# Kernel tuning notes

Hardware: AMD Instinct MI355X
Metric: run time of the kernel (lower is better)

The kernel has to match this reference:

```python
import jax, jax.numpy as jnp
import numpy as np

B, N, F, H, HEADS = 2, 256, 64, 64, 4
C = HEADS * H  # n_coefficients (coefficients_mlp is Identity => must equal n_heads*hidden)
EPS = 1e-5
INF = 1e5


def _lin(key, fan_in, fan_out, bias=True):
    k1, k2 = jax.random.split(key)
    w = jax.random.normal(k1, (fan_in, fan_out), jnp.float32) * (1.0 / np.sqrt(fan_in))
    if bias:
        b = jax.random.normal(k2, (fan_out,), jnp.float32) * 0.01
        return w, b
    return w


def setup_inputs() -> dict:
    key = jax.random.key(0)
    ks = jax.random.split(key, 16)
    inp = dict(
        h=jax.random.normal(ks[0], (B, N, F), jnp.float32),
        x=jax.random.normal(ks[1], (B, N, 3), jnp.float32),
        v=jax.random.normal(ks[2], (B, N, 3), jnp.float32),
    )
    inp['edge_w1'], inp['edge_b1'] = _lin(ks[3], 2 * F + 1, H)
    inp['edge_w2'], inp['edge_b2'] = _lin(ks[4], H, H)
    inp['sem_w'], inp['sem_b'] = _lin(ks[5], H, HEADS)
    inp['post_w1'], inp['post_b1'] = _lin(ks[6], C, H)
    inp['post_w2'], inp['post_b2'] = _lin(ks[7], H, H)
    inp['node_w1'], inp['node_b1'] = _lin(ks[8], C + H + F, H)
    inp['node_w2'], inp['node_b2'] = _lin(ks[9], H, F)
    inp['vel_w1'], inp['vel_b1'] = _lin(ks[10], F, H)
    inp['vel_w2'] = _lin(ks[11], H, 1, bias=False) * 0.001  # xavier gain=0.001 analogue
    inp['vmix_w'] = _lin(ks[12], C, 1, bias=False)[:, 0]
    inp['log_gamma'] = -jnp.log(jnp.linspace(1.0, 5.0, HEADS)).astype(jnp.float32)
    return inp


def reference(h, x, v, edge_w1, edge_b1, edge_w2, edge_b2, sem_w, sem_b,
              post_w1, post_b1, post_w2, post_b2, node_w1, node_b1,
              node_w2, node_b2, vel_w1, vel_b1, vel_w2, vmix_w, log_gamma):
    silu = jax.nn.silu
    n = h.shape[-2]
    eye = jnp.eye(n, dtype=h.dtype)[:, :, None]  # [N,N,1] diagonal mask

    # pairwise geometry: entry [i,j] = x_j - x_i
    x_minus_xt = x[..., None, :, :] - x[..., :, None, :]                # [B,N,N,3]
    x_norm = jnp.sqrt((x_minus_xt ** 2).sum(-1, keepdims=True) + EPS)   # [B,N,N,1]

    # pairwise node-feature concat (h_j, h_i) + distance -> edge MLP
    h_j = jnp.broadcast_to(h[..., None, :, :], (B, n, n, F))
    h_i = jnp.broadcast_to(h[..., :, None, :], (B, n, n, F))
    h_cat = jnp.concatenate([h_j, h_i, x_norm], axis=-1)                # [B,N,N,2F+1]
    h_e_mtx = silu(silu(h_cat @ edge_w1 + edge_b1) @ edge_w2 + edge_b2)  # [B,N,N,H]

    # euclidean attention: softmin over j of gamma*dist, diagonal masked out
    dist = (x_norm + INF * eye) * jnp.exp(log_gamma)                    # [B,N,N,heads]
    euclid_att = jax.nn.softmax(-dist, axis=-2)
    # semantic attention: LeakyReLU(0.2) logits, diagonal masked, softmax over j
    sem = jax.nn.leaky_relu(h_e_mtx @ sem_w + sem_b, 0.2) - INF * eye
    sem_att = jax.nn.softmax(sem, axis=-2)
    comb_att = jax.nn.softmax(euclid_att * sem_att, axis=-2)            # [B,N,N,heads]

    # attention-weighted edge features, flattened over (H, heads)
    h_e_att = (h_e_mtx[..., :, None] * comb_att[..., None, :]).reshape(B, n, n, C)

    # spatial attention (coefficients_mlp is Identity)
    unit = x_minus_xt / (x_norm + EPS)                                  # [B,N,N,3]
    # combinations.mean(dim=-3) without materializing [B,N,N,C,3]
    comb_sum = jnp.einsum('bijc,bijd->bicd', h_e_att, unit) / n         # [B,N,C,3]
    comb_norm = (comb_sum ** 2).sum(-1)                                 # [B,N,C]
    h_comb = silu(silu(comb_norm @ post_w1 + post_b1) @ post_w2 + post_b2)

    # delta_v = mean_j (v_mixing over C of combinations)
    delta_v = jnp.einsum('bijc,c,bijd->bid', h_e_att, vmix_w, unit) / n  # [B,N,3]

    h_agg = h_e_att.sum(axis=-2)                                        # sum over j -> [B,N,C]
    out = jnp.concatenate([h, h_agg, h_comb], axis=-1)
    out = silu(silu(out @ node_w1 + node_b1) @ node_w2 + node_b2)
    h_new = h + out                                                     # residual

    # coordinate / velocity update
    v_scale = silu(h_new @ vel_w1 + vel_b1) @ vel_w2                    # [B,N,1]
    v_new = delta_v + v_scale * v
    x_new = x + v_new
    return h_new, x_new, v_new
```

## Files before the change

kernel.cpp:

```cpp
#include <hip/hip_runtime.h>
#include <hip/hip_bf16.h>
#include <math.h>

#define EPSV 1e-5f
#define INFV 1e5f

typedef short bf16x8 __attribute__((ext_vector_type(8)));
typedef float f32x4 __attribute__((ext_vector_type(4)));

__device__ __forceinline__ float rcp_f(float x) { return __builtin_amdgcn_rcpf(x); }
__device__ __forceinline__ float silu_f(float v) { return v * rcp_f(1.0f + __expf(-v)); }

__device__ __forceinline__ unsigned short f2bf(float f) {
  unsigned int u = __float_as_uint(f);
  u = (u + 0x7fffu + ((u >> 16) & 1u)) >> 16;
  return (unsigned short)u;
}
__device__ __forceinline__ float bf2f(unsigned short h) {
  return __uint_as_float(((unsigned int)h) << 16);
}
__device__ __forceinline__ unsigned int pkbf(float a, float b) {
  float2 f2; f2.x = a; f2.y = b;
  __hip_bfloat162 t = __float22bfloat162_rn(f2);
  unsigned int u;
  __builtin_memcpy(&u, &t, 4);
  return u;
}

__device__ __forceinline__ void gemm64(const unsigned short* A_lds, const unsigned short* B_lds,
                                       int w, int l15, int quad, f32x4 acc[4][4]) {
#pragma unroll
  for (int tr = 0; tr < 4; ++tr)
#pragma unroll
    for (int tc = 0; tc < 4; ++tc)
      acc[tr][tc] = (f32x4){0.f, 0.f, 0.f, 0.f};
#pragma unroll
  for (int ms = 0; ms < 64; ms += 32) {
    bf16x8 af[4], bfr[4];
#pragma unroll
    for (int tr = 0; tr < 4; ++tr)
      af[tr] = *reinterpret_cast<const bf16x8*>(&A_lds[(64 * w + 16 * tr + l15) * 72 + ms + quad * 8]);
#pragma unroll
    for (int tc = 0; tc < 4; ++tc)
      bfr[tc] = *reinterpret_cast<const bf16x8*>(&B_lds[(16 * tc + l15) * 72 + ms + quad * 8]);
#pragma unroll
    for (int tr = 0; tr < 4; ++tr)
#pragma unroll
      for (int tc = 0; tc < 4; ++tc)
        acc[tr][tc] = __builtin_amdgcn_mfma_f32_16x16x32_bf16(af[tr], bfr[tc], acc[tr][tc], 0, 0, 0);
  }
}

__global__ __launch_bounds__(512, 2) void k_all(
    const float* __restrict__ h, const float* __restrict__ x, const float* __restrict__ v,
    const float* __restrict__ ew1, const float* __restrict__ eb1,
    const float* __restrict__ ew2, const float* __restrict__ eb2,
    const float* __restrict__ semw, const float* __restrict__ semb,
    const float* __restrict__ pw1, const float* __restrict__ pb1,
    const float* __restrict__ pw2, const float* __restrict__ pb2,
    const float* __restrict__ nw1, const float* __restrict__ nb1,
    const float* __restrict__ nw2, const float* __restrict__ nb2,
    const float* __restrict__ vw1, const float* __restrict__ vb1,
    const float* __restrict__ vw2, const float* __restrict__ vmix,
    const float* __restrict__ lgam, float* __restrict__ out) {

  __shared__ __align__(16) unsigned short TH0[256 * 72];
  __shared__ __align__(16) unsigned short TH1[256 * 72];
  __shared__ __align__(16) char R0[9216];
  __shared__ __align__(16) char R1[9216];
  __shared__ __align__(16) unsigned short E3T[16 * 72];
  __shared__ __align__(16) float4 unit_l[2][256];
  __shared__ float addk[2][64];
  __shared__ float w1dk[64];
  __shared__ __align__(16) float bms[512];

  const int bid = blockIdx.x;
  const int b   = bid >> 7;
  const int ip  = bid & 127;
  const int tid = threadIdx.x;
  const int g   = tid >> 8;
  const int jt  = tid & 255;
  const int i_g = 2 * ip + g;
  const int bi  = (b << 8) | i_g;
  const int bj  = (b << 8) | jt;

  const int w8   = tid >> 6;
  const int lid  = tid & 63;
  const int wg   = w8 & 3;
  const int l15  = lid & 15;
  const int quad = lid >> 4;

  unsigned short* E2Ta = (unsigned short*)R0;
  unsigned short* E2Tb = (unsigned short*)R1;
  unsigned short* THg  = g ? TH1 : TH0;
  char* Rg = g ? R1 : R0;
  float*  sd_g  = (float*)Rg;
  float4* cat_g = (float4*)Rg;
  float*  cn_g  = (float*)(Rg + 4096);
  float*  hag_g = (float*)(Rg + 5120);
  float4* scS   = (float4*)bms + g * 8;
  float4* scP   = (float4*)bms + 16 + g * 4;
  float4* scD   = (float4*)bms + 24 + g * 4;
  float*  dvs_g = bms + 128 + g * 4;

  const float xi0 = x[bi * 3 + 0], xi1 = x[bi * 3 + 1], xi2 = x[bi * 3 + 2];
  const float dx = x[bj * 3 + 0] - xi0;
  const float dy = x[bj * 3 + 1] - xi1;
  const float dz = x[bj * 3 + 2] - xi2;
  const float dn = sqrtf(dx * dx + dy * dy + dz * dz + EPSV);
  const float invn = rcp_f(dn + EPSV);
  const float ux = dx * invn, uy = dy * invn, uz = dz * invn;
  unit_l[g][jt] = make_float4(ux, uy, uz, dn);

  {
    const float4* hb4 = reinterpret_cast<const float4*>(h + (size_t)(b << 8) * 64);
#pragma unroll
    for (int q = 0; q < 8; ++q) {
      int idx = q * 512 + tid;
      float4 f4 = hb4[idx];
      int row = idx >> 4, c4 = idx & 15;
      uint2 pk;
      pk.x = pkbf(f4.x, f4.y);
      pk.y = pkbf(f4.z, f4.w);
      *reinterpret_cast<uint2*>(&TH0[row * 72 + c4 * 4]) = pk;
    }
  }
#pragma unroll
  for (int q = 0; q < 8; ++q) {
    int idx = q * 512 + tid;
    E2Ta[(idx & 63) * 72 + (idx >> 6)] = f2bf(ew1[idx]);
  }
#pragma unroll
  for (int q = 0; q < 8; ++q) {
    int idx = q * 512 + tid;
    E2Tb[(idx & 63) * 72 + (idx >> 6)] = f2bf(ew2[idx]);
  }
  {
    int n = tid >> 6, kk = tid & 63;
    E3T[n * 72 + kk] = f2bf((n < 4) ? semw[kk * 4 + n] : vmix[kk * 4 + (n - 4)]);
    E3T[(8 + n) * 72 + kk] = 0;
  }
  {
    int s = jt >> 6, k = jt & 63;
    const float* hrow = h + (size_t)bi * 64;
    float bp = 0.f;
#pragma unroll
    for (int f2 = 0; f2 < 16; ++f2) {
      int f = s * 16 + f2;
      bp += hrow[f] * ew1[(64 + f) * 64 + k];
    }
    bms[g * 256 + s * 64 + k] = bp;
  }
  __syncthreads();
  if (tid < 128) {
    int ii = tid >> 6, k = tid & 63;
    addk[ii][k] = eb1[k] + bms[ii * 256 + k] + bms[ii * 256 + 64 + k] +
                  bms[ii * 256 + 128 + k] + bms[ii * 256 + 192 + k];
  }
  if (tid < 64) w1dk[tid] = ew1[128 * 64 + tid];

  f32x4 acc1[2][4];
#pragma unroll
  for (int tr = 0; tr < 2; ++tr)
#pragma unroll
    for (int tc = 0; tc < 4; ++tc)
      acc1[tr][tc] = (f32x4){0.f, 0.f, 0.f, 0.f};
#pragma unroll
  for (int ms = 0; ms < 64; ms += 32) {
    bf16x8 af[2], bfr[4];
#pragma unroll
    for (int tr = 0; tr < 2; ++tr)
      af[tr] = *reinterpret_cast<const bf16x8*>(&TH0[(32 * w8 + 16 * tr + l15) * 72 + ms + quad * 8]);
#pragma unroll
    for (int tc = 0; tc < 4; ++tc)
      bfr[tc] = *reinterpret_cast<const bf16x8*>(&E2Ta[(16 * tc + l15) * 72 + ms + quad * 8]);
#pragma unroll
    for (int tr = 0; tr < 2; ++tr)
#pragma unroll
      for (int tc = 0; tc < 4; ++tc)
        acc1[tr][tc] = __builtin_amdgcn_mfma_f32_16x16x32_bf16(af[tr], bfr[tc], acc1[tr][tc], 0, 0, 0);
  }
  __syncthreads();

#pragma unroll
  for (int tc = 0; tc < 4; ++tc) {
    float wd  = w1dk[16 * tc + l15];
    float ak0 = addk[0][16 * tc + l15];
    float ak1 = addk[1][16 * tc + l15];
#pragma unroll
    for (int tr = 0; tr < 2; ++tr)
#pragma unroll
      for (int r = 0; r < 4; ++r) {
        int row = 32 * w8 + 16 * tr + quad * 4 + r;
        float a = acc1[tr][tc][r];
        float d0 = unit_l[0][row].w, d1 = unit_l[1][row].w;
        TH0[row * 72 + 16 * tc + l15] = f2bf(silu_f(a + ak0 + d0 * wd));
        TH1[row * 72 + 16 * tc + l15] = f2bf(silu_f(a + ak1 + d1 * wd));
      }
  }
  __syncthreads();

  f32x4 acc2[4][4];
  gemm64(THg, E2Tb, wg, l15, quad, acc2);
  __syncthreads();
#pragma unroll
  for (int tc = 0; tc < 4; ++tc) {
    float b2 = eb2[16 * tc + l15];
#pragma unroll
    for (int tr = 0; tr < 4; ++tr)
#pragma unroll
      for (int r = 0; r < 4; ++r) {
        int row = 64 * wg + 16 * tr + quad * 4 + r;
        THg[row * 72 + 16 * tc + l15] = f2bf(silu_f(acc2[tr][tc][r] + b2));
      }
  }
  __syncthreads();

  f32x4 acc3[4];
#pragma unroll
  for (int tr = 0; tr < 4; ++tr) acc3[tr] = (f32x4){0.f, 0.f, 0.f, 0.f};
#pragma unroll
  for (int ms = 0; ms < 64; ms += 32) {
    bf16x8 b3 = *reinterpret_cast<const bf16x8*>(&E3T[l15 * 72 + ms + quad * 8]);
#pragma unroll
    for (int tr = 0; tr < 4; ++tr) {
      bf16x8 a3 = *reinterpret_cast<const bf16x8*>(&THg[(64 * wg + 16 * tr + l15) * 72 + ms + quad * 8]);
      acc3[tr] = __builtin_amdgcn_mfma_f32_16x16x32_bf16(a3, b3, acc3[tr], 0, 0, 0);
    }
  }
  if (l15 < 8) {
#pragma unroll
    for (int tr = 0; tr < 4; ++tr)
#pragma unroll
      for (int r = 0; r < 4; ++r)
        sd_g[(64 * wg + 16 * tr + quad * 4 + r) * 8 + l15] = acc3[tr][r];
  }
  __syncthreads();

  float4 s01 = *reinterpret_cast<const float4*>(sd_g + jt * 8);
  float4 s23 = *reinterpret_cast<const float4*>(sd_g + jt * 8 + 4);
  float4 sbv = *reinterpret_cast<const float4*>(semb);
  const float diag = (jt == i_g) ? INFV : 0.0f;
  float4 sl;
  sl.x = s01.x + sbv.x; sl.y = s01.y + sbv.y; sl.z = s01.z + sbv.z; sl.w = s01.w + sbv.w;
  sl.x = ((sl.x > 0.f) ? sl.x : 0.2f * sl.x) - diag;
  sl.y = ((sl.y > 0.f) ? sl.y : 0.2f * sl.y) - diag;
  sl.z = ((sl.z > 0.f) ? sl.z : 0.2f * sl.z) - diag;
  sl.w = ((sl.w > 0.f) ? sl.w : 0.2f * sl.w) - diag;

  float4 lg4 = *reinterpret_cast<const float4*>(lgam);
  const float dni = dn + diag;
  float4 e_eu = make_float4(__expf(-dni * __expf(lg4.x)), __expf(-dni * __expf(lg4.y)),
                            __expf(-dni * __expf(lg4.z)), __expf(-dni * __expf(lg4.w)));
  float4 e_sem = make_float4(__expf(sl.x), __expf(sl.y), __expf(sl.z), __expf(sl.w));

  float4 a8 = e_eu, b8 = e_sem;
#pragma unroll
  for (int off = 32; off >= 1; off >>= 1) {
    a8.x += __shfl_xor(a8.x, off); a8.y += __shfl_xor(a8.y, off);
    a8.z += __shfl_xor(a8.z, off); a8.w += __shfl_xor(a8.w, off);
    b8.x += __shfl_xor(b8.x, off); b8.y += __shfl_xor(b8.y, off);
    b8.z += __shfl_xor(b8.z, off); b8.w += __shfl_xor(b8.w, off);
  }
  if (lid == 0) { scS[wg] = a8; scS[4 + wg] = b8; }
  __syncthreads();
  float4 Se, Ss;
  {
    float4 r0 = scS[0], r1 = scS[1], r2 = scS[2], r3 = scS[3];
    Se = make_float4(r0.x + r1.x + r2.x + r3.x, r0.y + r1.y + r2.y + r3.y,
                     r0.z + r1.z + r2.z + r3.z, r0.w + r1.w + r2.w + r3.w);
    float4 s0 = scS[4], s1 = scS[5], s2 = scS[6], s3 = scS[7];
    Ss = make_float4(s0.x + s1.x + s2.x + s3.x, s0.y + s1.y + s2.y + s3.y,
                     s0.z + s1.z + s2.z + s3.z, s0.w + s1.w + s2.w + s3.w);
  }

  float4 p = make_float4((e_eu.x * rcp_f(Se.x)) * (e_sem.x * rcp_f(Ss.x)),
                         (e_eu.y * rcp_f(Se.y)) * (e_sem.y * rcp_f(Ss.y)),
                         (e_eu.z * rcp_f(Se.z)) * (e_sem.z * rcp_f(Ss.z)),
                         (e_eu.w * rcp_f(Se.w)) * (e_sem.w * rcp_f(Ss.w)));
  float4 ep = make_float4(__expf(p.x), __expf(p.y), __expf(p.z), __expf(p.w));
  float4 sp8 = ep;
#pragma unroll
  for (int off = 32; off >= 1; off >>= 1) {
    sp8.x += __shfl_xor(sp8.x, off); sp8.y += __shfl_xor(sp8.y, off);
    sp8.z += __shfl_xor(sp8.z, off); sp8.w += __shfl_xor(sp8.w, off);
  }
  if (lid == 0) scP[wg] = sp8;
  __syncthreads();
  float4 Sp;
  {
    float4 r0 = scP[0], r1 = scP[1], r2 = scP[2], r3 = scP[3];
    Sp = make_float4(r0.x + r1.x + r2.x + r3.x, r0.y + r1.y + r2.y + r3.y,
                     r0.z + r1.z + r2.z + r3.z, r0.w + r1.w + r2.w + r3.w);
  }
  float4 catt = make_float4(ep.x * rcp_f(Sp.x), ep.y * rcp_f(Sp.y),
                            ep.z * rcp_f(Sp.z), ep.w * rcp_f(Sp.w));
  cat_g[jt] = catt;

  float s = catt.x * s23.x + catt.y * s23.y + catt.z * s23.z + catt.w * s23.w;
  float dvx = s * ux, dvy = s * uy, dvz = s * uz;
#pragma unroll
  for (int off = 32; off >= 1; off >>= 1) {
    dvx += __shfl_xor(dvx, off); dvy += __shfl_xor(dvy, off); dvz += __shfl_xor(dvz, off);
  }
  if (lid == 0) scD[wg] = make_float4(dvx, dvy, dvz, 0.f);
  __syncthreads();
  if (jt == 0) {
    float4 r0 = scD[0], r1 = scD[1], r2 = scD[2], r3 = scD[3];
    const float inv = 1.0f / 256.0f;
    dvs_g[0] = (r0.x + r1.x + r2.x + r3.x) * inv;
    dvs_g[1] = (r0.y + r1.y + r2.y + r3.y) * inv;
    dvs_g[2] = (r0.z + r1.z + r2.z + r3.z) * inv;
  }

  {
    const int kk = lid & 15;
    const int jq = lid >> 4;
    const int k  = 16 * wg + kk;
    float agg[4] = {0.f, 0.f, 0.f, 0.f};
    float ax[4]  = {0.f, 0.f, 0.f, 0.f};
    float ay[4]  = {0.f, 0.f, 0.f, 0.f};
    float az[4]  = {0.f, 0.f, 0.f, 0.f};
#pragma unroll 4
    for (int jr2 = 0; jr2 < 64; ++jr2) {
      int jj = jq * 64 + ((jr2 + 4 * jq) & 63);
      float hev = bf2f(THg[jj * 72 + k]);
      float4 ca = cat_g[jj];
      float4 u  = unit_l[g][jj];
      float w0 = hev * ca.x, w1 = hev * ca.y, w2 = hev * ca.z, w3 = hev * ca.w;
      agg[0] += w0; agg[1] += w1; agg[2] += w2; agg[3] += w3;
      ax[0] += w0 * u.x; ay[0] += w0 * u.y; az[0] += w0 * u.z;
      ax[1] += w1 * u.x; ay[1] += w1 * u.y; az[1] += w1 * u.z;
      ax[2] += w2 * u.x; ay[2] += w2 * u.y; az[2] += w2 * u.z;
      ax[3] += w3 * u.x; ay[3] += w3 * u.y; az[3] += w3 * u.z;
    }
#pragma unroll
    for (int off = 16; off <= 32; off <<= 1) {
#pragma unroll
      for (int hd = 0; hd < 4; ++hd) {
        agg[hd] += __shfl_xor(agg[hd], off);
        ax[hd]  += __shfl_xor(ax[hd], off);
        ay[hd]  += __shfl_xor(ay[hd], off);
        az[hd]  += __shfl_xor(az[hd], off);
      }
    }
    if (jq == 0) {
      const float inv = 1.0f / 256.0f;
#pragma unroll
      for (int hd = 0; hd < 4; ++hd) {
        float cx = ax[hd] * inv, cy = ay[hd] * inv, cz = az[hd] * inv;
        cn_g[k * 4 + hd]  = cx * cx + cy * cy + cz * cz;
        hag_g[k * 4 + hd] = agg[hd];
      }
    }
  }
  __syncthreads();

  {
    const int k = lid;
    float* tmpg = (float*)THg;
    float a1 = 0.f;
#pragma unroll 16
    for (int m2 = 0; m2 < 64; ++m2) {
      int m = 64 * wg + m2;
      a1 += cn_g[m] * pw1[m * 64 + k];
    }
    tmpg[wg * 64 + k] = a1;
    if (wg == 1 || wg == 2) {
      float a2 = 0.f;
      int base = (wg - 1) * 128;
#pragma unroll 16
      for (int m2 = 0; m2 < 128; ++m2) {
        int m = base + m2;
        a2 += hag_g[m] * nw1[(64 + m) * 64 + k];
      }
      tmpg[256 + (wg - 1) * 64 + k] = a2;
    } else if (wg == 3) {
      float a2 = 0.f;
      const float* hrow = h + (size_t)bi * 64;
#pragma unroll 16
      for (int m = 0; m < 64; ++m) a2 += hrow[m] * nw1[m * 64 + k];
      tmpg[384 + k] = a2;
    }
  }
  __syncthreads();

  if (wg == 0) {
    const int k = lid;
    float* tmpg = (float*)THg;
    float* sh2  = tmpg + 512;

    float m1 = silu_f(pb1[k] + tmpg[k] + tmpg[64 + k] + tmpg[128 + k] + tmpg[192 + k]);
    sh2[k] = m1;

    float a = 0.f;
#pragma unroll 16
    for (int m = 0; m < 64; ++m) a += sh2[m] * pw2[m * 64 + k];
    float hcomb = silu_f(pb2[k] + a);
    sh2[64 + k] = hcomb;

    a = nb1[k] + tmpg[256 + k] + tmpg[320 + k] + tmpg[384 + k];
#pragma unroll 16
    for (int m = 0; m < 64; ++m) a += sh2[64 + m] * nw1[(320 + m) * 64 + k];
    sh2[128 + k] = silu_f(a);

    a = 0.f;
#pragma unroll 16
    for (int m = 0; m < 64; ++m) a += sh2[128 + m] * nw2[m * 64 + k];
    float hn = h[(size_t)bi * 64 + k] + silu_f(nb2[k] + a);
    out[(size_t)bi * 64 + k] = hn;
    sh2[192 + k] = hn;

    a = 0.f;
#pragma unroll 16
    for (int m = 0; m < 64; ++m) a += sh2[192 + m] * vw1[m * 64 + k];
    float vh = silu_f(vb1[k] + a) * vw2[k];
#pragma unroll
    for (int off = 32; off >= 1; off >>= 1) vh += __shfl_xor(vh, off);

    if (k == 0) {
      const float xi[3] = {xi0, xi1, xi2};
#pragma unroll
      for (int d = 0; d < 3; ++d) {
        float vn = dvs_g[d] + vh * v[bi * 3 + d];
        out[32768 + bi * 3 + d] = xi[d] + vn;
        out[34304 + bi * 3 + d] = vn;
      }
    }
  }
}

extern "C" void kernel_launch(void* const* d_in, const int* in_sizes, int n_in,
                              void* d_out, int out_size, void* d_ws, size_t ws_size,
                              hipStream_t stream) {
  const float* h    = (const float*)d_in[0];
  const float* x    = (const float*)d_in[1];
  const float* v    = (const float*)d_in[2];
  const float* ew1  = (const float*)d_in[3];
  const float* eb1  = (const float*)d_in[4];
  const float* ew2  = (const float*)d_in[5];
  const float* eb2  = (const float*)d_in[6];
  const float* semw = (const float*)d_in[7];
  const float* semb = (const float*)d_in[8];
  const float* pw1  = (const float*)d_in[9];
  const float* pb1  = (const float*)d_in[10];
  const float* pw2  = (const float*)d_in[11];
  const float* pb2  = (const float*)d_in[12];
  const float* nw1  = (const float*)d_in[13];
  const float* nb1  = (const float*)d_in[14];
  const float* nw2  = (const float*)d_in[15];
  const float* nb2  = (const float*)d_in[16];
  const float* vw1  = (const float*)d_in[17];
  const float* vb1  = (const float*)d_in[18];
  const float* vw2  = (const float*)d_in[19];
  const float* vmix = (const float*)d_in[20];
  const float* lgam = (const float*)d_in[21];
  float* out = (float*)d_out;

  k_all<<<256, 512, 0, stream>>>(h, x, v, ew1, eb1, ew2, eb2, semw, semb,
                                 pw1, pb1, pw2, pb2, nw1, nb1, nw2, nb2,
                                 vw1, vb1, vw2, vmix, lgam, out);
}
```

Measured before the change: 126.7 us.

## Drop redundant block barriers and vectorize the per-head aggregation loop

Removes four __syncthreads between the edge-MLP stages. Each wave only reads and writes its own rows there, so the barriers are not needed. Adds a separate SD1 buffer so the second group's semantic scores no longer alias the E2Tb weights that other waves may still be reading. Folds the addk bias precompute into the epilogue reads from bms. The aggregation loop now gives each thread four k columns and loads them with one ushort4, at the cost of more accumulator registers and extra shuffle-reduction steps.

```diff
diff --git a/kernel.cpp b/kernel.cpp
--- a/kernel.cpp
+++ b/kernel.cpp
@@ -68,10 +68,11 @@
   __shared__ __align__(16) unsigned short TH1[256 * 72];
   __shared__ __align__(16) char R0[9216];
   __shared__ __align__(16) char R1[9216];
+  __shared__ __align__(16) float SD1[2048];
   __shared__ __align__(16) unsigned short E3T[16 * 72];
   __shared__ __align__(16) float4 unit_l[2][256];
-  __shared__ float addk[2][64];
   __shared__ float w1dk[64];
+  __shared__ float eb1l[64];
   __shared__ __align__(16) float bms[512];
 
   const int bid = blockIdx.x;
@@ -94,7 +95,7 @@
   unsigned short* E2Tb = (unsigned short*)R1;
   unsigned short* THg  = g ? TH1 : TH0;
   char* Rg = g ? R1 : R0;
-  float*  sd_g  = (float*)Rg;
+  float*  sd_g  = g ? SD1 : (float*)R0;
   float4* cat_g = (float4*)Rg;
   float*  cn_g  = (float*)(Rg + 4096);
   float*  hag_g = (float*)(Rg + 5120);
@@ -140,6 +141,7 @@
     E3T[n * 72 + kk] = f2bf((n < 4) ? semw[kk * 4 + n] : vmix[kk * 4 + (n - 4)]);
     E3T[(8 + n) * 72 + kk] = 0;
   }
+  if (tid < 64) { w1dk[tid] = ew1[128 * 64 + tid]; eb1l[tid] = eb1[tid]; }
   {
     int s = jt >> 6, k = jt & 63;
     const float* hrow = h + (size_t)bi * 64;
@@ -152,12 +154,6 @@
     bms[g * 256 + s * 64 + k] = bp;
   }
   __syncthreads();
-  if (tid < 128) {
-    int ii = tid >> 6, k = tid & 63;
-    addk[ii][k] = eb1[k] + bms[ii * 256 + k] + bms[ii * 256 + 64 + k] +
-                  bms[ii * 256 + 128 + k] + bms[ii * 256 + 192 + k];
-  }
-  if (tid < 64) w1dk[tid] = ew1[128 * 64 + tid];
 
   f32x4 acc1[2][4];
 #pragma unroll
@@ -180,13 +176,14 @@
       for (int tc = 0; tc < 4; ++tc)
         acc1[tr][tc] = __builtin_amdgcn_mfma_f32_16x16x32_bf16(af[tr], bfr[tc], acc1[tr][tc], 0, 0, 0);
   }
-  __syncthreads();
 
 #pragma unroll
   for (int tc = 0; tc < 4; ++tc) {
-    float wd  = w1dk[16 * tc + l15];
-    float ak0 = addk[0][16 * tc + l15];
-    float ak1 = addk[1][16 * tc + l15];
+    int kc = 16 * tc + l15;
+    float wd = w1dk[kc];
+    float eb = eb1l[kc];
+    float ak0 = eb + bms[kc] + bms[64 + kc] + bms[128 + kc] + bms[192 + kc];
+    float ak1 = eb + bms[256 + kc] + bms[320 + kc] + bms[384 + kc] + bms[448 + kc];
 #pragma unroll
     for (int tr = 0; tr < 2; ++tr)
 #pragma unroll
@@ -194,15 +191,14 @@
         int row = 32 * w8 + 16 * tr + quad * 4 + r;
         float a = acc1[tr][tc][r];
         float d0 = unit_l[0][row].w, d1 = unit_l[1][row].w;
-        TH0[row * 72 + 16 * tc + l15] = f2bf(silu_f(a + ak0 + d0 * wd));
-        TH1[row * 72 + 16 * tc + l15] = f2bf(silu_f(a + ak1 + d1 * wd));
+        TH0[row * 72 + kc] = f2bf(silu_f(a + ak0 + d0 * wd));
+        TH1[row * 72 + kc] = f2bf(silu_f(a + ak1 + d1 * wd));
       }
   }
   __syncthreads();
 
   f32x4 acc2[4][4];
   gemm64(THg, E2Tb, wg, l15, quad, acc2);
-  __syncthreads();
 #pragma unroll
   for (int tc = 0; tc < 4; ++tc) {
     float b2 = eb2[16 * tc + l15];
@@ -214,7 +210,6 @@
         THg[row * 72 + 16 * tc + l15] = f2bf(silu_f(acc2[tr][tc][r] + b2));
       }
   }
-  __syncthreads();
 
   f32x4 acc3[4];
 #pragma unroll
@@ -235,7 +230,6 @@
       for (int r = 0; r < 4; ++r)
         sd_g[(64 * wg + 16 * tr + quad * 4 + r) * 8 + l15] = acc3[tr][r];
   }
-  __syncthreads();
 
   float4 s01 = *reinterpret_cast<const float4*>(sd_g + jt * 8);
   float4 s23 = *reinterpret_cast<const float4*>(sd_g + jt * 8 + 4);
@@ -314,43 +308,58 @@
   }
 
   {
-    const int kk = lid & 15;
-    const int jq = lid >> 4;
-    const int k  = 16 * wg + kk;
-    float agg[4] = {0.f, 0.f, 0.f, 0.f};
-    float ax[4]  = {0.f, 0.f, 0.f, 0.f};
-    float ay[4]  = {0.f, 0.f, 0.f, 0.f};
-    float az[4]  = {0.f, 0.f, 0.f, 0.f};
+    const int jg   = lid >> 2;
+    const int ksub = lid & 3;
+    const int kb   = 16 * wg + 4 * ksub;
+    float agg[4][4], ax[4][4], ay[4][4], az[4][4];
+#pragma unroll
+    for (int kk = 0; kk < 4; ++kk)
+#pragma unroll
+      for (int hd = 0; hd < 4; ++hd) {
+        agg[kk][hd] = 0.f; ax[kk][hd] = 0.f; ay[kk][hd] = 0.f; az[kk][hd] = 0.f;
+      }
 #pragma unroll 4
-    for (int jr2 = 0; jr2 < 64; ++jr2) {
-      int jj = jq * 64 + ((jr2 + 4 * jq) & 63);
-      float hev = bf2f(THg[jj * 72 + k]);
+    for (int jr = 0; jr < 16; ++jr) {
+      int jj = jr * 16 + jg;
+      ushort4 hv4 = *reinterpret_cast<const ushort4*>(&THg[jj * 72 + kb]);
       float4 ca = cat_g[jj];
       float4 u  = unit_l[g][jj];
-      float w0 = hev * ca.x, w1 = hev * ca.y, w2 = hev * ca.z, w3 = hev * ca.w;
-      agg[0] += w0; agg[1] += w1; agg[2] += w2; agg[3] += w3;
-      ax[0] += w0 * u.x; ay[0] += w0 * u.y; az[0] += w0 * u.z;
-      ax[1] += w1 * u.x; ay[1] += w1 * u.y; az[1] += w1 * u.z;
-      ax[2] += w2 * u.x; ay[2] += w2 * u.y; az[2] += w2 * u.z;
-      ax[3] += w3 * u.x; ay[3] += w3 * u.y; az[3] += w3 * u.z;
-    }
-#pragma unroll
-    for (int off = 16; off <= 32; off <<= 1) {
-#pragma unroll
-      for (int hd = 0; hd < 4; ++hd) {
-        agg[hd] += __shfl_xor(agg[hd], off);
-        ax[hd]  += __shfl_xor(ax[hd], off);
-        ay[hd]  += __shfl_xor(ay[hd], off);
-        az[hd]  += __shfl_xor(az[hd], off);
-      }
-    }
-    if (jq == 0) {
+      float hev[4] = { bf2f(hv4.x), bf2f(hv4.y), bf2f(hv4.z), bf2f(hv4.w) };
+#pragma unroll
+      for (int kk = 0; kk < 4; ++kk) {
+        float c0 = hev[kk] * ca.x, c1 = hev[kk] * ca.y, c2 = hev[kk] * ca.z, c3 = hev[kk] * ca.w;
+        agg[kk][0] += c0; agg[kk][1] += c1; agg[kk][2] += c2; agg[kk][3] += c3;
+        ax[kk][0] += c0 * u.x; ay[kk][0] += c0 * u.y; az[kk][0] += c0 * u.z;
+        ax[kk][1] += c1 * u.x; ay[kk][1] += c1 * u.y; az[kk][1] += c1 * u.z;
+        ax[kk][2] += c2 * u.x; ay[kk][2] += c2 * u.y; az[kk][2] += c2 * u.z;
+        ax[kk][3] += c3 * u.x; ay[kk][3] += c3 * u.y; az[kk][3] += c3 * u.z;
+      }
+    }
+#pragma unroll
+    for (int off = 4; off <= 32; off <<= 1)
+#pragma unroll
+      for (int kk = 0; kk < 4; ++kk)
+#pragma unroll
+        for (int hd = 0; hd < 4; ++hd) {
+          agg[kk][hd] += __shfl_xor(agg[kk][hd], off);
+          ax[kk][hd]  += __shfl_xor(ax[kk][hd], off);
+          ay[kk][hd]  += __shfl_xor(ay[kk][hd], off);
+          az[kk][hd]  += __shfl_xor(az[kk][hd], off);
+        }
+    if (jg == 0) {
       const float inv = 1.0f / 256.0f;
 #pragma unroll
-      for (int hd = 0; hd < 4; ++hd) {
-        float cx = ax[hd] * inv, cy = ay[hd] * inv, cz = az[hd] * inv;
-        cn_g[k * 4 + hd]  = cx * cx + cy * cy + cz * cz;
-        hag_g[k * 4 + hd] = agg[hd];
+      for (int kk = 0; kk < 4; ++kk) {
+        int k = kb + kk;
+        f32x4 cnv, hgv;
+#pragma unroll
+        for (int hd = 0; hd < 4; ++hd) {
+          float cx = ax[kk][hd] * inv, cy = ay[kk][hd] * inv, cz = az[kk][hd] * inv;
+          cnv[hd] = cx * cx + cy * cy + cz * cz;
+          hgv[hd] = agg[kk][hd];
+        }
+        *reinterpret_cast<f32x4*>(&cn_g[k * 4])  = cnv;
+        *reinterpret_cast<f32x4*>(&hag_g[k * 4]) = hgv;
       }
     }
   }
```

After: 127.1 us. No clear change (+0.3%).
